# Kernel optimization log

Measured on AMD Instinct MI355X. Metric: run time of the kernel, lower is better.

Reference implementation:

```python
import jax, jax.numpy as jnp
import numpy as np

N, E = 50000, 800000
F_IN, H, P, C = 128, 64, 16, 40
L = 3  # gcn_layers


def setup_inputs() -> dict:
    key = jax.random.key(0)
    ks = jax.random.split(key, 10)
    s = 0.05
    return {
        "x_h": jax.random.normal(ks[0], (N, F_IN), jnp.float32),
        "pos_feat": jax.random.normal(ks[1], (N, P), jnp.float32),
        "edge_index": jax.random.randint(ks[2], (2, E), 0, N, dtype=jnp.int32),
        "W_pos": jax.random.normal(ks[3], (P, H), jnp.float32) * s,
        "b_pos": jnp.zeros((H,), jnp.float32),
        "W_init": jax.random.normal(ks[4], (F_IN, H), jnp.float32) * s,
        "b_init": jnp.zeros((H,), jnp.float32),
        "W_l": jax.random.normal(ks[5], (L, H, H), jnp.float32) * s,  # neighbor weight
        "W_r": jax.random.normal(ks[6], (L, H, H), jnp.float32) * s,  # root weight
        "b_conv": jnp.zeros((L, H), jnp.float32),
        "W_last": jax.random.normal(ks[7], (H, C), jnp.float32) * s,
        "b_last": jnp.zeros((C,), jnp.float32),
    }


def _sage_conv(x, src, dst, Wl, Wr, b):
    # PyG SAGEConv(aggr='mean'): out_i = Wl @ mean_{j in N(i)} x_j + Wr @ x_i + b
    msgs = x[src]  # [E, H] gather of source-node features
    agg = jax.ops.segment_sum(msgs, dst, num_segments=N)
    cnt = jax.ops.segment_sum(jnp.ones((E,), x.dtype), dst, num_segments=N)
    agg = agg / jnp.clip(cnt, 1.0, None)[:, None]  # mean; deg-0 nodes -> 0
    return agg @ Wl + x @ Wr + b


def reference(x_h, pos_feat, edge_index, W_pos, b_pos, W_init, b_init,
              W_l, W_r, b_conv, W_last, b_last):
    src, dst = edge_index[0], edge_index[1]
    # pos_embedding -> (hyperbolic encode simplified to identity in Euclidean manifold) -> tanh
    hyp_pos = jnp.tanh(pos_feat @ W_pos + b_pos)  # [N, H]
    h = x_h @ W_init + b_init  # [N, H]
    for i in range(L):
        h = _sage_conv(h, src, dst, W_l[i], W_r[i], b_conv[i])
        if i != L - 1:
            h = h + hyp_pos       # run_base == 'False' branch
            h = jax.nn.relu(h)    # dropout is no-op in eval mode
    emb = h @ W_last + b_last     # [N, C]
    return emb, jax.nn.log_softmax(emb, axis=1)
```

## Files before the change

### kernel.cpp

```cpp
#include <hip/hip_runtime.h>
#include <hip/hip_bf16.h>

#define NN 50000
#define NE 800000
#define FIN 128
#define HD 64
#define NC 40
#define XG   782
#define XG2  781
#define NB   391
#define NBK  782
#define BW   64
#define BSTR 2048

typedef __hip_bfloat16 bf16;
typedef __attribute__((ext_vector_type(8))) short bf16x8;
typedef __attribute__((ext_vector_type(4))) float f32x4;

__device__ __forceinline__ void acc8(float* a, uint4 v){
  a[0] += __uint_as_float(v.x << 16); a[1] += __uint_as_float(v.x & 0xffff0000u);
  a[2] += __uint_as_float(v.y << 16); a[3] += __uint_as_float(v.y & 0xffff0000u);
  a[4] += __uint_as_float(v.z << 16); a[5] += __uint_as_float(v.z & 0xffff0000u);
  a[6] += __uint_as_float(v.w << 16); a[7] += __uint_as_float(v.w & 0xffff0000u);
}

__device__ __forceinline__ unsigned pack2(float lo, float hi){
  union { bf16 b; unsigned short u; } a, b;
  a.b = __float2bfloat16(lo);
  b.b = __float2bfloat16(hi);
  return (unsigned)a.u | ((unsigned)b.u << 16);
}

__device__ __forceinline__ short f2bf_bits(float f){
  union { bf16 b; short s; } u;
  u.b = __float2bfloat16(f);
  return u.s;
}

__device__ __forceinline__ void init_body(
    int wid, const float* __restrict__ x, const float* __restrict__ pos,
    const float* __restrict__ Wi, const float* __restrict__ bi,
    const float* __restrict__ Wp, const float* __restrict__ bp,
    bf16* __restrict__ h0b, bf16* __restrict__ hypb, int lane){
  const int quad = lane >> 4;
  const int col  = lane & 15;
  const int nw   = XG * 4;

  bf16x8 wif[4][4];
  #pragma unroll
  for (int ct = 0; ct < 4; ++ct)
    #pragma unroll
    for (int kf = 0; kf < 4; ++kf)
      #pragma unroll
      for (int j = 0; j < 8; ++j)
        wif[ct][kf][j] = f2bf_bits(Wi[(kf*32 + quad*8 + j)*HD + ct*16 + col]);
  bf16x8 wpf[4];
  #pragma unroll
  for (int ct = 0; ct < 4; ++ct)
    #pragma unroll
    for (int j = 0; j < 8; ++j){
      const int k = quad*8 + j;
      wpf[ct][j] = (k < 16) ? f2bf_bits(Wp[k*HD + ct*16 + col]) : (short)0;
    }
  float bih[4], bph[4];
  #pragma unroll
  for (int c = 0; c < 4; ++c){ bih[c] = bi[c*16 + col]; bph[c] = bp[c*16 + col]; }

  for (int t = wid; t < NN/16; t += nw){
    const int n0 = t * 16;
    bf16x8 af[4];
    #pragma unroll
    for (int kf = 0; kf < 4; ++kf){
      const float* xr = x + (size_t)(n0 + col)*FIN + kf*32 + quad*8;
      const float4 f0 = *(const float4*)xr;
      const float4 f1 = *(const float4*)(xr + 4);
      af[kf][0] = f2bf_bits(f0.x); af[kf][1] = f2bf_bits(f0.y);
      af[kf][2] = f2bf_bits(f0.z); af[kf][3] = f2bf_bits(f0.w);
      af[kf][4] = f2bf_bits(f1.x); af[kf][5] = f2bf_bits(f1.y);
      af[kf][6] = f2bf_bits(f1.z); af[kf][7] = f2bf_bits(f1.w);
    }
    bf16x8 ap;
    #pragma unroll
    for (int j = 0; j < 8; ++j) ap[j] = 0;
    if (quad < 2){
      const float* pr = pos + (size_t)(n0 + col)*16 + quad*8;
      const float4 p0 = *(const float4*)pr;
      const float4 p1 = *(const float4*)(pr + 4);
      ap[0] = f2bf_bits(p0.x); ap[1] = f2bf_bits(p0.y);
      ap[2] = f2bf_bits(p0.z); ap[3] = f2bf_bits(p0.w);
      ap[4] = f2bf_bits(p1.x); ap[5] = f2bf_bits(p1.y);
      ap[6] = f2bf_bits(p1.z); ap[7] = f2bf_bits(p1.w);
    }
    f32x4 ah[4], app[4];
    #pragma unroll
    for (int c = 0; c < 4; ++c){
      ah[c]  = (f32x4){bih[c], bih[c], bih[c], bih[c]};
      app[c] = (f32x4){bph[c], bph[c], bph[c], bph[c]};
    }
    #pragma unroll
    for (int ct = 0; ct < 4; ++ct){
      #pragma unroll
      for (int kf = 0; kf < 4; ++kf)
        ah[ct] = __builtin_amdgcn_mfma_f32_16x16x32_bf16(af[kf], wif[ct][kf], ah[ct], 0, 0, 0);
      app[ct] = __builtin_amdgcn_mfma_f32_16x16x32_bf16(ap, wpf[ct], app[ct], 0, 0, 0);
    }
    #pragma unroll
    for (int reg = 0; reg < 4; ++reg){
      const int n = n0 + quad*4 + reg;
      #pragma unroll
      for (int c = 0; c < 4; ++c){
        h0b[(size_t)n*HD + c*16 + col]  = __float2bfloat16(ah[c][reg]);
        hypb[(size_t)n*HD + c*16 + col] = __float2bfloat16(tanhf(app[c][reg]));
      }
    }
  }
}

__device__ __forceinline__ void xform_body(
    int wid, int nw, const bf16* __restrict__ h, const float* __restrict__ Wl,
    const float* __restrict__ Wr, const float* __restrict__ bc,
    const bf16* __restrict__ hypb, const int use_hyp,
    bf16* __restrict__ y, bf16* __restrict__ z, int lane){
  const int quad = lane >> 4;
  const int col  = lane & 15;

  bf16x8 bfr[8][2];
  #pragma unroll
  for (int ct = 0; ct < 8; ++ct){
    const float* W = (ct < 4) ? Wl : Wr;
    const int nc = (ct & 3) * 16 + col;
    #pragma unroll
    for (int kf = 0; kf < 2; ++kf)
      #pragma unroll
      for (int j = 0; j < 8; ++j)
        bfr[ct][kf][j] = f2bf_bits(W[(kf*32 + quad*8 + j)*HD + nc]);
  }
  float zb[4];
  #pragma unroll
  for (int c = 0; c < 4; ++c) zb[c] = bc[c*16 + col];

  for (int t = wid; t < NN/16; t += nw){
    const int n0 = t * 16;
    union { uint4 u; bf16x8 v; } a0, a1;
    a0.u = *(const uint4*)(h + (size_t)(n0 + col)*HD + quad*8);
    a1.u = *(const uint4*)(h + (size_t)(n0 + col)*HD + 32 + quad*8);
    f32x4 acc[8];
    #pragma unroll
    for (int c = 0; c < 4; ++c) acc[c] = (f32x4){0.f, 0.f, 0.f, 0.f};
    #pragma unroll
    for (int c = 0; c < 4; ++c) acc[4+c] = (f32x4){zb[c], zb[c], zb[c], zb[c]};
    #pragma unroll
    for (int ct = 0; ct < 8; ++ct){
      acc[ct] = __builtin_amdgcn_mfma_f32_16x16x32_bf16(a0.v, bfr[ct][0], acc[ct], 0, 0, 0);
      acc[ct] = __builtin_amdgcn_mfma_f32_16x16x32_bf16(a1.v, bfr[ct][1], acc[ct], 0, 0, 0);
    }
    #pragma unroll
    for (int reg = 0; reg < 4; ++reg){
      const int n = n0 + quad*4 + reg;
      #pragma unroll
      for (int c = 0; c < 4; ++c){
        y[(size_t)n*HD + c*16 + col] = __float2bfloat16(acc[c][reg]);
        float zv = acc[4+c][reg];
        if (use_hyp) zv += __bfloat162float(hypb[(size_t)n*HD + c*16 + col]);
        z[(size_t)n*HD + c*16 + col] = __float2bfloat16(zv);
      }
    }
  }
}

__global__ __launch_bounds__(256) void k_hist(
    const int* __restrict__ ei, int* __restrict__ histT,
    const float* __restrict__ x, const float* __restrict__ pos,
    const float* __restrict__ Wi, const float* __restrict__ bi,
    const float* __restrict__ Wp, const float* __restrict__ bp,
    bf16* __restrict__ h0b, bf16* __restrict__ hypb){
  __shared__ int lh[NBK];
  if (blockIdx.x < NB){
    for (int i = threadIdx.x; i < NBK; i += 256) lh[i] = 0;
    __syncthreads();
    int e = blockIdx.x * 2048 + threadIdx.x;
    #pragma unroll
    for (int j = 0; j < 8; ++j, e += 256)
      if (e < NE) atomicAdd(&lh[ei[NE + e] >> 6], 1);
    __syncthreads();
    for (int i = threadIdx.x; i < NBK; i += 256)
      histT[blockIdx.x*NBK + i] = lh[i];
    return;
  }
  init_body((blockIdx.x - NB) * 4 + (threadIdx.x >> 6),
            x, pos, Wi, bi, Wp, bp, h0b, hypb, threadIdx.x & 63);
}

__global__ __launch_bounds__(512) void k_scanA(
    const int* __restrict__ histT, int* __restrict__ ofsT,
    int* __restrict__ totals){
  __shared__ int sc[512];
  const int b = blockIdx.x;
  const int t = threadIdx.x;
  const int v = (t < NB) ? histT[t*NBK + b] : 0;
  sc[t] = v; __syncthreads();
  for (int off = 1; off < 512; off <<= 1){
    const int xv = (t >= off) ? sc[t - off] : 0;
    __syncthreads();
    sc[t] += xv;
    __syncthreads();
  }
  if (t < NB) ofsT[t*NBK + b] = sc[t] - v;
  if (t == 511) totals[b] = sc[511];
}

__global__ __launch_bounds__(256) void k_scatter(
    const int* __restrict__ ei, const int* __restrict__ ofsT,
    int* __restrict__ packed){
  __shared__ int cur[NBK];
  for (int i = threadIdx.x; i < NBK; i += 256)
    cur[i] = (i << 11) + ofsT[blockIdx.x*NBK + i];
  __syncthreads();
  int e = blockIdx.x * 2048 + threadIdx.x;
  #pragma unroll
  for (int j = 0; j < 8; ++j, e += 256){
    if (e < NE){
      const int d = ei[NE + e];
      const int s = ei[e];
      const int b = d >> 6;
      const int p = atomicAdd(&cur[b], 1);
      if (p < ((b + 1) << 11))
        packed[p] = s | ((d & 63) << 16);
    }
  }
}

__global__ __launch_bounds__(256) void k_ellx(
    const int* __restrict__ packed, const int* __restrict__ totals,
    unsigned short* __restrict__ esrc, int* __restrict__ degp,
    const bf16* __restrict__ h0, const float* __restrict__ Wl,
    const float* __restrict__ Wr, const float* __restrict__ bc,
    const bf16* __restrict__ hypb, bf16* __restrict__ y, bf16* __restrict__ z){
  if (blockIdx.x < NBK){
    __shared__ int cnt[BW];
    __shared__ unsigned short ell[BW * 64];
    if (threadIdx.x < BW) cnt[threadIdx.x] = 0;
    __syncthreads();
    const int b  = blockIdx.x;
    const int lo = b << 11;
    const int hi = lo + totals[b];
    for (int e = lo + threadIdx.x; e < hi; e += 256){
      const int pk = packed[e];
      const int dl = (pk >> 16) & 63;
      const int p  = atomicAdd(&cnt[dl], 1);
      if (p < 64) ell[dl*64 + p] = (unsigned short)(pk & 0xffff);
    }
    __syncthreads();
    const int n0 = b * BW;
    for (int i = threadIdx.x; i < BW * 8; i += 256){
      const int node = i >> 3;
      if (n0 + node < NN)
        ((uint4*)(esrc + (size_t)(n0 + node)*64))[i & 7] = ((const uint4*)ell)[i];
    }
    for (int i = threadIdx.x; i < BW; i += 256)
      if (n0 + i < NN) degp[n0 + i] = cnt[i];
    return;
  }
  xform_body((blockIdx.x - NBK)*4 + (threadIdx.x >> 6), XG2*4,
             h0, Wl, Wr, bc, hypb, 1, y, z, threadIdx.x & 63);
}

__device__ __forceinline__ void gather_stage(
    const bf16* __restrict__ y, const bf16* __restrict__ z,
    const int* __restrict__ degp, const unsigned short* __restrict__ esrc,
    unsigned int* hs, const int do_relu){
  const int lane = threadIdx.x & 63;
  const int w    = threadIdx.x >> 6;
  const int grp  = lane >> 3;
  const int fq   = lane & 7;
  const int nl   = (w << 3) + grp;
  const int n    = (blockIdx.x << 5) + nl;
  const int ns   = (n < NN) ? n : 0;
  const int deg  = (n < NN) ? min(degp[n], 64) : 0;
  const uint4* er = (const uint4*)(esrc + ((size_t)ns << 6));
  float a[8] = {0,0,0,0,0,0,0,0};
  for (int eb = 0; eb < 64; eb += 8){
    if (!__any(eb < deg)) break;
    union { uint4 u; unsigned short s[8]; } ev;
    ev.u = er[eb >> 3];
    const int m = deg - eb;
    #pragma unroll
    for (int j = 0; j < 8; ++j){
      if (j < m){
        const uint4 v = ((const uint4*)(y + (size_t)ev.s[j]*HD))[fq];
        acc8(a, v);
      }
    }
  }
  const float inv = deg > 0 ? 1.f / (float)deg : 0.f;
  const uint4 zv = ((const uint4*)(z + (size_t)ns*HD))[fq];
  float zf[8];
  zf[0] = __uint_as_float(zv.x << 16); zf[1] = __uint_as_float(zv.x & 0xffff0000u);
  zf[2] = __uint_as_float(zv.y << 16); zf[3] = __uint_as_float(zv.y & 0xffff0000u);
  zf[4] = __uint_as_float(zv.z << 16); zf[5] = __uint_as_float(zv.z & 0xffff0000u);
  zf[6] = __uint_as_float(zv.w << 16); zf[7] = __uint_as_float(zv.w & 0xffff0000u);
  float o[8];
  #pragma unroll
  for (int j = 0; j < 8; ++j){
    o[j] = a[j]*inv + zf[j];
    if (do_relu) o[j] = fmaxf(o[j], 0.f);
  }
  uint4 pv;
  pv.x = pack2(o[0], o[1]);
  pv.y = pack2(o[2], o[3]);
  pv.z = pack2(o[4], o[5]);
  pv.w = pack2(o[6], o[7]);
  *(uint4*)(hs + nl*32 + ((fq ^ (nl & 7)) << 2)) = pv;
}

__device__ __forceinline__ bf16x8 lds_frag(const unsigned int* hs, int r, int slotlin){
  union { uint4 u; bf16x8 v; } t;
  t.u = *(const uint4*)(hs + r*32 + ((slotlin ^ (r & 7)) << 2));
  return t.v;
}

__global__ __launch_bounds__(256) void k_gx(
    const bf16* __restrict__ y, const bf16* __restrict__ z,
    const int* __restrict__ degp, const unsigned short* __restrict__ esrc,
    const float* __restrict__ Wl, const float* __restrict__ Wr,
    const float* __restrict__ bc, const bf16* __restrict__ hypb,
    const int use_hyp, bf16* __restrict__ yo, bf16* __restrict__ zo){
  __shared__ unsigned int hs[32*32];
  const int lane = threadIdx.x & 63;
  const int w    = threadIdx.x >> 6;
  const int quad = lane >> 4;
  const int col  = lane & 15;
  const int tile = w & 1;
  const int ch   = w >> 1;

  bf16x8 fl[2][2], fr[2][2];
  float zb[2];
  #pragma unroll
  for (int c = 0; c < 2; ++c){
    const int nc = (ch*2 + c)*16 + col;
    zb[c] = bc[nc];
    #pragma unroll
    for (int kf = 0; kf < 2; ++kf)
      #pragma unroll
      for (int j = 0; j < 8; ++j){
        fl[c][kf][j] = f2bf_bits(Wl[(kf*32 + quad*8 + j)*HD + nc]);
        fr[c][kf][j] = f2bf_bits(Wr[(kf*32 + quad*8 + j)*HD + nc]);
      }
  }

  gather_stage(y, z, degp, esrc, hs, 1);
  __syncthreads();

  const int r = tile*16 + col;
  const bf16x8 a0 = lds_frag(hs, r, quad);
  const bf16x8 a1 = lds_frag(hs, r, quad + 4);
  f32x4 ay[2], az[2];
  #pragma unroll
  for (int c = 0; c < 2; ++c){
    ay[c] = (f32x4){0.f, 0.f, 0.f, 0.f};
    az[c] = (f32x4){zb[c], zb[c], zb[c], zb[c]};
    ay[c] = __builtin_amdgcn_mfma_f32_16x16x32_bf16(a0, fl[c][0], ay[c], 0, 0, 0);
    ay[c] = __builtin_amdgcn_mfma_f32_16x16x32_bf16(a1, fl[c][1], ay[c], 0, 0, 0);
    az[c] = __builtin_amdgcn_mfma_f32_16x16x32_bf16(a0, fr[c][0], az[c], 0, 0, 0);
    az[c] = __builtin_amdgcn_mfma_f32_16x16x32_bf16(a1, fr[c][1], az[c], 0, 0, 0);
  }
  const int n0b = blockIdx.x << 5;
  #pragma unroll
  for (int reg = 0; reg < 4; ++reg){
    const int n = n0b + tile*16 + quad*4 + reg;
    if (n < NN){
      #pragma unroll
      for (int c = 0; c < 2; ++c){
        const int oc = (ch*2 + c)*16 + col;
        yo[(size_t)n*HD + oc] = __float2bfloat16(ay[c][reg]);
        float zv = az[c][reg];
        if (use_hyp) zv += __bfloat162float(hypb[(size_t)n*HD + oc]);
        zo[(size_t)n*HD + oc] = __float2bfloat16(zv);
      }
    }
  }
}

__global__ __launch_bounds__(256) void k_gf(
    const bf16* __restrict__ y, const bf16* __restrict__ z,
    const int* __restrict__ degp, const unsigned short* __restrict__ esrc,
    const float* __restrict__ Wl, const float* __restrict__ bl,
    float* __restrict__ out){
  __shared__ unsigned int hs[32*32];
  const int lane = threadIdx.x & 63;
  const int w    = threadIdx.x >> 6;
  const int quad = lane >> 4;
  const int col  = lane & 15;

  bf16x8 wf[3][2];
  float bb[3];
  #pragma unroll
  for (int ct = 0; ct < 3; ++ct){
    const int nc = ct*16 + col;
    const bool valid = nc < NC;
    bb[ct] = valid ? bl[nc] : -1e30f;
    #pragma unroll
    for (int kf = 0; kf < 2; ++kf)
      #pragma unroll
      for (int j = 0; j < 8; ++j)
        wf[ct][kf][j] = valid ? f2bf_bits(Wl[(kf*32 + quad*8 + j)*NC + nc]) : (short)0;
  }

  gather_stage(y, z, degp, esrc, hs, 0);
  __syncthreads();
  if (w >= 2) return;

  const int tile = w;
  const int r = tile*16 + col;
  const bf16x8 a0 = lds_frag(hs, r, quad);
  const bf16x8 a1 = lds_frag(hs, r, quad + 4);
  f32x4 acc[3];
  #pragma unroll
  for (int ct = 0; ct < 3; ++ct){
    acc[ct] = (f32x4){bb[ct], bb[ct], bb[ct], bb[ct]};
    acc[ct] = __builtin_amdgcn_mfma_f32_16x16x32_bf16(a0, wf[ct][0], acc[ct], 0, 0, 0);
    acc[ct] = __builtin_amdgcn_mfma_f32_16x16x32_bf16(a1, wf[ct][1], acc[ct], 0, 0, 0);
  }
  const int n0b = blockIdx.x << 5;
  #pragma unroll
  for (int reg = 0; reg < 4; ++reg){
    const float e0 = acc[0][reg], e1 = acc[1][reg], e2 = acc[2][reg];
    float vmax = fmaxf(fmaxf(e0, e1), e2);
    vmax = fmaxf(vmax, __shfl_xor(vmax, 1, 64));
    vmax = fmaxf(vmax, __shfl_xor(vmax, 2, 64));
    vmax = fmaxf(vmax, __shfl_xor(vmax, 4, 64));
    vmax = fmaxf(vmax, __shfl_xor(vmax, 8, 64));
    float s = __expf(e0 - vmax) + __expf(e1 - vmax) + __expf(e2 - vmax);
    s += __shfl_xor(s, 1, 64);
    s += __shfl_xor(s, 2, 64);
    s += __shfl_xor(s, 4, 64);
    s += __shfl_xor(s, 8, 64);
    const float off = vmax + __logf(s);
    const int n = n0b + tile*16 + quad*4 + reg;
    if (n < NN){
      #pragma unroll
      for (int ct = 0; ct < 3; ++ct){
        const int nc = ct*16 + col;
        if (nc < NC){
          const float e = acc[ct][reg];
          out[(size_t)n*NC + nc]                 = e;
          out[(size_t)NN*NC + (size_t)n*NC + nc] = e - off;
        }
      }
    }
  }
}

extern "C" void kernel_launch(void* const* d_in, const int* in_sizes, int n_in,
                              void* d_out, int out_size, void* d_ws, size_t ws_size,
                              hipStream_t stream){
  (void)in_sizes; (void)n_in; (void)out_size; (void)ws_size;
  const float* x_h    = (const float*)d_in[0];
  const float* pos    = (const float*)d_in[1];
  const int*   ei     = (const int*)  d_in[2];
  const float* W_pos  = (const float*)d_in[3];
  const float* b_pos  = (const float*)d_in[4];
  const float* W_init = (const float*)d_in[5];
  const float* b_init = (const float*)d_in[6];
  const float* W_l    = (const float*)d_in[7];
  const float* W_r    = (const float*)d_in[8];
  const float* b_conv = (const float*)d_in[9];
  const float* W_last = (const float*)d_in[10];
  const float* b_last = (const float*)d_in[11];
  float* out = (float*)d_out;

  char* p = (char*)d_ws;
  auto alloc = [&](size_t bytes)->char*{
    char* r = p; p += (bytes + 255) & ~(size_t)255; return r;
  };
  bf16* hb0  = (bf16*)alloc((size_t)NN*HD*2);
  bf16* y0   = (bf16*)alloc((size_t)NN*HD*2);
  bf16* z0   = (bf16*)alloc((size_t)NN*HD*2);
  bf16* y1   = (bf16*)alloc((size_t)NN*HD*2);
  bf16* z1   = (bf16*)alloc((size_t)NN*HD*2);
  bf16* hypb = (bf16*)alloc((size_t)NN*HD*2);
  unsigned short* esrc = (unsigned short*)alloc((size_t)NN*64*2);
  int* degp   = (int*)alloc((size_t)NN*4);
  int* histT  = (int*)alloc((size_t)NB*NBK*4);
  int* ofsT   = (int*)alloc((size_t)NB*NBK*4);
  int* totals = (int*)alloc((size_t)NBK*4);
  int* packed = (int*)alloc((size_t)NBK*BSTR*4);

  k_hist   <<<NB + XG, 256, 0, stream>>>(ei, histT, x_h, pos,
                                         W_init, b_init, W_pos, b_pos, hb0, hypb);
  k_scanA  <<<NBK, 512, 0, stream>>>(histT, ofsT, totals);
  k_scatter<<<NB, 256, 0, stream>>>(ei, ofsT, packed);
  k_ellx   <<<NBK + XG2, 256, 0, stream>>>(packed, totals, esrc, degp,
                                           hb0, W_l, W_r, b_conv, hypb, y0, z0);
  k_gx <<<1563, 256, 0, stream>>>(y0, z0, degp, esrc,
                                  W_l + 1*HD*HD, W_r + 1*HD*HD, b_conv + 1*HD,
                                  hypb, 1, y1, z1);
  k_gx <<<1563, 256, 0, stream>>>(y1, z1, degp, esrc,
                                  W_l + 2*HD*HD, W_r + 2*HD*HD, b_conv + 2*HD,
                                  hypb, 0, y0, z0);
  k_gf <<<1563, 256, 0, stream>>>(y0, z0, degp, esrc, W_last, b_last, out);
}
```

Baseline: 249.4 us.

## Aggregate raw features then apply fused concat GEMM instead of pre-transforming y/z

Reorders each SAGE layer to gather-mean the raw node features first, then run one MFMA GEMM over the concatenated [mean, self] row with stacked Wl/Wr, adding hyp and applying ReLU in the epilogue. This removes the separate y/z transform pass: each layer reads and writes one feature buffer instead of two, and the transform no longer sits in k_ellx. The final kernel also fuses the layer-3 conv with the output projection and log-softmax. The cost is a doubled K dimension in each block's GEMM, extra LDS staging, and another block-level barrier.

```diff
diff --git a/kernel.cpp b/kernel.cpp
--- a/kernel.cpp
+++ b/kernel.cpp
@@ -7,11 +7,11 @@
 #define HD 64
 #define NC 40
 #define XG   782
-#define XG2  781
 #define NB   391
 #define NBK  782
 #define BW   64
 #define BSTR 2048
+#define GGRID 1563
 
 typedef __hip_bfloat16 bf16;
 typedef __attribute__((ext_vector_type(8))) short bf16x8;
@@ -111,58 +111,6 @@
       for (int c = 0; c < 4; ++c){
         h0b[(size_t)n*HD + c*16 + col]  = __float2bfloat16(ah[c][reg]);
         hypb[(size_t)n*HD + c*16 + col] = __float2bfloat16(tanhf(app[c][reg]));
-      }
-    }
-  }
-}
-
-__device__ __forceinline__ void xform_body(
-    int wid, int nw, const bf16* __restrict__ h, const float* __restrict__ Wl,
-    const float* __restrict__ Wr, const float* __restrict__ bc,
-    const bf16* __restrict__ hypb, const int use_hyp,
-    bf16* __restrict__ y, bf16* __restrict__ z, int lane){
-  const int quad = lane >> 4;
-  const int col  = lane & 15;
-
-  bf16x8 bfr[8][2];
-  #pragma unroll
-  for (int ct = 0; ct < 8; ++ct){
-    const float* W = (ct < 4) ? Wl : Wr;
-    const int nc = (ct & 3) * 16 + col;
-    #pragma unroll
-    for (int kf = 0; kf < 2; ++kf)
-      #pragma unroll
-      for (int j = 0; j < 8; ++j)
-        bfr[ct][kf][j] = f2bf_bits(W[(kf*32 + quad*8 + j)*HD + nc]);
-  }
-  float zb[4];
-  #pragma unroll
-  for (int c = 0; c < 4; ++c) zb[c] = bc[c*16 + col];
-
-  for (int t = wid; t < NN/16; t += nw){
-    const int n0 = t * 16;
-    union { uint4 u; bf16x8 v; } a0, a1;
-    a0.u = *(const uint4*)(h + (size_t)(n0 + col)*HD + quad*8);
-    a1.u = *(const uint4*)(h + (size_t)(n0 + col)*HD + 32 + quad*8);
-    f32x4 acc[8];
-    #pragma unroll
-    for (int c = 0; c < 4; ++c) acc[c] = (f32x4){0.f, 0.f, 0.f, 0.f};
-    #pragma unroll
-    for (int c = 0; c < 4; ++c) acc[4+c] = (f32x4){zb[c], zb[c], zb[c], zb[c]};
-    #pragma unroll
-    for (int ct = 0; ct < 8; ++ct){
-      acc[ct] = __builtin_amdgcn_mfma_f32_16x16x32_bf16(a0.v, bfr[ct][0], acc[ct], 0, 0, 0);
-      acc[ct] = __builtin_amdgcn_mfma_f32_16x16x32_bf16(a1.v, bfr[ct][1], acc[ct], 0, 0, 0);
-    }
-    #pragma unroll
-    for (int reg = 0; reg < 4; ++reg){
-      const int n = n0 + quad*4 + reg;
-      #pragma unroll
-      for (int c = 0; c < 4; ++c){
-        y[(size_t)n*HD + c*16 + col] = __float2bfloat16(acc[c][reg]);
-        float zv = acc[4+c][reg];
-        if (use_hyp) zv += __bfloat162float(hypb[(size_t)n*HD + c*16 + col]);
-        z[(size_t)n*HD + c*16 + col] = __float2bfloat16(zv);
       }
     }
   }
@@ -230,45 +178,43 @@
   }
 }
 
-__global__ __launch_bounds__(256) void k_ellx(
+__global__ __launch_bounds__(256) void k_ell(
     const int* __restrict__ packed, const int* __restrict__ totals,
-    unsigned short* __restrict__ esrc, int* __restrict__ degp,
-    const bf16* __restrict__ h0, const float* __restrict__ Wl,
-    const float* __restrict__ Wr, const float* __restrict__ bc,
-    const bf16* __restrict__ hypb, bf16* __restrict__ y, bf16* __restrict__ z){
-  if (blockIdx.x < NBK){
-    __shared__ int cnt[BW];
-    __shared__ unsigned short ell[BW * 64];
-    if (threadIdx.x < BW) cnt[threadIdx.x] = 0;
-    __syncthreads();
-    const int b  = blockIdx.x;
-    const int lo = b << 11;
-    const int hi = lo + totals[b];
-    for (int e = lo + threadIdx.x; e < hi; e += 256){
-      const int pk = packed[e];
-      const int dl = (pk >> 16) & 63;
-      const int p  = atomicAdd(&cnt[dl], 1);
-      if (p < 64) ell[dl*64 + p] = (unsigned short)(pk & 0xffff);
-    }
-    __syncthreads();
-    const int n0 = b * BW;
-    for (int i = threadIdx.x; i < BW * 8; i += 256){
-      const int node = i >> 3;
-      if (n0 + node < NN)
-        ((uint4*)(esrc + (size_t)(n0 + node)*64))[i & 7] = ((const uint4*)ell)[i];
-    }
-    for (int i = threadIdx.x; i < BW; i += 256)
-      if (n0 + i < NN) degp[n0 + i] = cnt[i];
-    return;
-  }
-  xform_body((blockIdx.x - NBK)*4 + (threadIdx.x >> 6), XG2*4,
-             h0, Wl, Wr, bc, hypb, 1, y, z, threadIdx.x & 63);
-}
-
-__device__ __forceinline__ void gather_stage(
-    const bf16* __restrict__ y, const bf16* __restrict__ z,
-    const int* __restrict__ degp, const unsigned short* __restrict__ esrc,
-    unsigned int* hs, const int do_relu){
+    unsigned short* __restrict__ esrc, int* __restrict__ degp){
+  __shared__ int cnt[BW];
+  __shared__ unsigned short ell[BW * 64];
+  if (threadIdx.x < BW) cnt[threadIdx.x] = 0;
+  __syncthreads();
+  const int b  = blockIdx.x;
+  const int lo = b << 11;
+  const int hi = lo + totals[b];
+  for (int e = lo + threadIdx.x; e < hi; e += 256){
+    const int pk = packed[e];
+    const int dl = (pk >> 16) & 63;
+    const int p  = atomicAdd(&cnt[dl], 1);
+    if (p < 64) ell[dl*64 + p] = (unsigned short)(pk & 0xffff);
+  }
+  __syncthreads();
+  const int n0 = b * BW;
+  for (int i = threadIdx.x; i < BW * 8; i += 256){
+    const int node = i >> 3;
+    if (n0 + node < NN)
+      ((uint4*)(esrc + (size_t)(n0 + node)*64))[i & 7] = ((const uint4*)ell)[i];
+  }
+  for (int i = threadIdx.x; i < BW; i += 256)
+    if (n0 + i < NN) degp[n0 + i] = min(cnt[i], 64);
+}
+
+
+__device__ __forceinline__ bf16x8 lds_frag(const unsigned int* hs, int r, int slot){
+  union { uint4 u; bf16x8 v; } t;
+  t.u = *(const uint4*)(hs + r*32 + ((slot ^ (r & 7)) << 2));
+  return t.v;
+}
+
+__device__ __forceinline__ void gather_own_stage(
+    const bf16* __restrict__ h, const int* __restrict__ degp,
+    const unsigned short* __restrict__ esrc, unsigned int* hs){
   const int lane = threadIdx.x & 63;
   const int w    = threadIdx.x >> 6;
   const int grp  = lane >> 3;
@@ -277,6 +223,10 @@
   const int n    = (blockIdx.x << 5) + nl;
   const int ns   = (n < NN) ? n : 0;
   const int deg  = (n < NN) ? min(degp[n], 64) : 0;
+
+  const uint4 hv = ((const uint4*)(h + (size_t)ns*HD))[fq];
+  *(uint4*)(hs + 1024 + nl*32 + ((fq ^ (nl & 7)) << 2)) = hv;
+
   const uint4* er = (const uint4*)(esrc + ((size_t)ns << 6));
   float a[8] = {0,0,0,0,0,0,0,0};
   for (int eb = 0; eb < 64; eb += 8){
@@ -287,45 +237,27 @@
     #pragma unroll
     for (int j = 0; j < 8; ++j){
       if (j < m){
-        const uint4 v = ((const uint4*)(y + (size_t)ev.s[j]*HD))[fq];
+        const uint4 v = ((const uint4*)(h + (size_t)ev.s[j]*HD))[fq];
         acc8(a, v);
       }
     }
   }
   const float inv = deg > 0 ? 1.f / (float)deg : 0.f;
-  const uint4 zv = ((const uint4*)(z + (size_t)ns*HD))[fq];
-  float zf[8];
-  zf[0] = __uint_as_float(zv.x << 16); zf[1] = __uint_as_float(zv.x & 0xffff0000u);
-  zf[2] = __uint_as_float(zv.y << 16); zf[3] = __uint_as_float(zv.y & 0xffff0000u);
-  zf[4] = __uint_as_float(zv.z << 16); zf[5] = __uint_as_float(zv.z & 0xffff0000u);
-  zf[6] = __uint_as_float(zv.w << 16); zf[7] = __uint_as_float(zv.w & 0xffff0000u);
-  float o[8];
-  #pragma unroll
-  for (int j = 0; j < 8; ++j){
-    o[j] = a[j]*inv + zf[j];
-    if (do_relu) o[j] = fmaxf(o[j], 0.f);
-  }
   uint4 pv;
-  pv.x = pack2(o[0], o[1]);
-  pv.y = pack2(o[2], o[3]);
-  pv.z = pack2(o[4], o[5]);
-  pv.w = pack2(o[6], o[7]);
+  pv.x = pack2(a[0]*inv, a[1]*inv);
+  pv.y = pack2(a[2]*inv, a[3]*inv);
+  pv.z = pack2(a[4]*inv, a[5]*inv);
+  pv.w = pack2(a[6]*inv, a[7]*inv);
   *(uint4*)(hs + nl*32 + ((fq ^ (nl & 7)) << 2)) = pv;
 }
 
-__device__ __forceinline__ bf16x8 lds_frag(const unsigned int* hs, int r, int slotlin){
-  union { uint4 u; bf16x8 v; } t;
-  t.u = *(const uint4*)(hs + r*32 + ((slotlin ^ (r & 7)) << 2));
-  return t.v;
-}
-
-__global__ __launch_bounds__(256) void k_gx(
-    const bf16* __restrict__ y, const bf16* __restrict__ z,
-    const int* __restrict__ degp, const unsigned short* __restrict__ esrc,
+__global__ __launch_bounds__(256) void k_g(
+    const bf16* __restrict__ h, const int* __restrict__ degp,
+    const unsigned short* __restrict__ esrc,
     const float* __restrict__ Wl, const float* __restrict__ Wr,
     const float* __restrict__ bc, const bf16* __restrict__ hypb,
-    const int use_hyp, bf16* __restrict__ yo, bf16* __restrict__ zo){
-  __shared__ unsigned int hs[32*32];
+    bf16* __restrict__ ho){
+  __shared__ unsigned int hs[2048];
   const int lane = threadIdx.x & 63;
   const int w    = threadIdx.x >> 6;
   const int quad = lane >> 4;
@@ -333,64 +265,127 @@
   const int tile = w & 1;
   const int ch   = w >> 1;
 
-  bf16x8 fl[2][2], fr[2][2];
+  bf16x8 fw[2][4];
   float zb[2];
   #pragma unroll
   for (int c = 0; c < 2; ++c){
     const int nc = (ch*2 + c)*16 + col;
     zb[c] = bc[nc];
     #pragma unroll
-    for (int kf = 0; kf < 2; ++kf)
+    for (int kf = 0; kf < 4; ++kf)
       #pragma unroll
       for (int j = 0; j < 8; ++j){
-        fl[c][kf][j] = f2bf_bits(Wl[(kf*32 + quad*8 + j)*HD + nc]);
-        fr[c][kf][j] = f2bf_bits(Wr[(kf*32 + quad*8 + j)*HD + nc]);
+        const int k = kf*32 + quad*8 + j;
+        fw[c][kf][j] = f2bf_bits((k < 64) ? Wl[k*HD + nc] : Wr[(k - 64)*HD + nc]);
       }
   }
 
-  gather_stage(y, z, degp, esrc, hs, 1);
+  gather_own_stage(h, degp, esrc, hs);
   __syncthreads();
 
   const int r = tile*16 + col;
   const bf16x8 a0 = lds_frag(hs, r, quad);
   const bf16x8 a1 = lds_frag(hs, r, quad + 4);
-  f32x4 ay[2], az[2];
+  const bf16x8 a2 = lds_frag(hs + 1024, r, quad);
+  const bf16x8 a3 = lds_frag(hs + 1024, r, quad + 4);
+  __syncthreads();
+
+  const int n0b = blockIdx.x << 5;
+  unsigned short* st = (unsigned short*)hs;
+  f32x4 acc[2];
   #pragma unroll
   for (int c = 0; c < 2; ++c){
-    ay[c] = (f32x4){0.f, 0.f, 0.f, 0.f};
-    az[c] = (f32x4){zb[c], zb[c], zb[c], zb[c]};
-    ay[c] = __builtin_amdgcn_mfma_f32_16x16x32_bf16(a0, fl[c][0], ay[c], 0, 0, 0);
-    ay[c] = __builtin_amdgcn_mfma_f32_16x16x32_bf16(a1, fl[c][1], ay[c], 0, 0, 0);
-    az[c] = __builtin_amdgcn_mfma_f32_16x16x32_bf16(a0, fr[c][0], az[c], 0, 0, 0);
-    az[c] = __builtin_amdgcn_mfma_f32_16x16x32_bf16(a1, fr[c][1], az[c], 0, 0, 0);
-  }
-  const int n0b = blockIdx.x << 5;
+    acc[c] = (f32x4){zb[c], zb[c], zb[c], zb[c]};
+    acc[c] = __builtin_amdgcn_mfma_f32_16x16x32_bf16(a0, fw[c][0], acc[c], 0, 0, 0);
+    acc[c] = __builtin_amdgcn_mfma_f32_16x16x32_bf16(a1, fw[c][1], acc[c], 0, 0, 0);
+    acc[c] = __builtin_amdgcn_mfma_f32_16x16x32_bf16(a2, fw[c][2], acc[c], 0, 0, 0);
+    acc[c] = __builtin_amdgcn_mfma_f32_16x16x32_bf16(a3, fw[c][3], acc[c], 0, 0, 0);
+  }
   #pragma unroll
   for (int reg = 0; reg < 4; ++reg){
-    const int n = n0b + tile*16 + quad*4 + reg;
-    if (n < NN){
-      #pragma unroll
-      for (int c = 0; c < 2; ++c){
-        const int oc = (ch*2 + c)*16 + col;
-        yo[(size_t)n*HD + oc] = __float2bfloat16(ay[c][reg]);
-        float zv = az[c][reg];
-        if (use_hyp) zv += __bfloat162float(hypb[(size_t)n*HD + oc]);
-        zo[(size_t)n*HD + oc] = __float2bfloat16(zv);
-      }
-    }
-  }
+    const int rr = tile*16 + quad*4 + reg;
+    const int nn = n0b + rr;
+    #pragma unroll
+    for (int c = 0; c < 2; ++c){
+      const int oc = (ch*2 + c)*16 + col;
+      float v = acc[c][reg];
+      if (nn < NN) v += __bfloat162float(hypb[(size_t)nn*HD + oc]);
+      v = fmaxf(v, 0.f);
+      st[rr*64 + (((oc >> 3) ^ (rr & 7)) << 3) + (oc & 7)] = (unsigned short)f2bf_bits(v);
+    }
+  }
+  __syncthreads();
+  const int grp = lane >> 3;
+  const int fq  = lane & 7;
+  const int nl  = (w << 3) + grp;
+  const int n   = n0b + nl;
+  if (n < NN)
+    ((uint4*)(ho + (size_t)n*HD))[fq] = *(const uint4*)(hs + nl*32 + ((fq ^ (nl & 7)) << 2));
 }
 
 __global__ __launch_bounds__(256) void k_gf(
-    const bf16* __restrict__ y, const bf16* __restrict__ z,
-    const int* __restrict__ degp, const unsigned short* __restrict__ esrc,
-    const float* __restrict__ Wl, const float* __restrict__ bl,
+    const bf16* __restrict__ h, const int* __restrict__ degp,
+    const unsigned short* __restrict__ esrc,
+    const float* __restrict__ Wl, const float* __restrict__ Wr,
+    const float* __restrict__ bc,
+    const float* __restrict__ Wlast, const float* __restrict__ blast,
     float* __restrict__ out){
-  __shared__ unsigned int hs[32*32];
+  __shared__ unsigned int hs[2048];
   const int lane = threadIdx.x & 63;
   const int w    = threadIdx.x >> 6;
   const int quad = lane >> 4;
   const int col  = lane & 15;
+  const int tile = w & 1;
+  const int ch   = w >> 1;
+
+  bf16x8 fw[2][4];
+  float zb[2];
+  #pragma unroll
+  for (int c = 0; c < 2; ++c){
+    const int nc = (ch*2 + c)*16 + col;
+    zb[c] = bc[nc];
+    #pragma unroll
+    for (int kf = 0; kf < 4; ++kf)
+      #pragma unroll
+      for (int j = 0; j < 8; ++j){
+        const int k = kf*32 + quad*8 + j;
+        fw[c][kf][j] = f2bf_bits((k < 64) ? Wl[k*HD + nc] : Wr[(k - 64)*HD + nc]);
+      }
+  }
+
+  gather_own_stage(h, degp, esrc, hs);
+  __syncthreads();
+
+  const int r = tile*16 + col;
+  const bf16x8 a0 = lds_frag(hs, r, quad);
+  const bf16x8 a1 = lds_frag(hs, r, quad + 4);
+  const bf16x8 a2 = lds_frag(hs + 1024, r, quad);
+  const bf16x8 a3 = lds_frag(hs + 1024, r, quad + 4);
+  __syncthreads();
+
+  const int n0b = blockIdx.x << 5;
+  unsigned short* st = (unsigned short*)hs;
+  f32x4 acc[2];
+  #pragma unroll
+  for (int c = 0; c < 2; ++c){
+    acc[c] = (f32x4){zb[c], zb[c], zb[c], zb[c]};
+    acc[c] = __builtin_amdgcn_mfma_f32_16x16x32_bf16(a0, fw[c][0], acc[c], 0, 0, 0);
+    acc[c] = __builtin_amdgcn_mfma_f32_16x16x32_bf16(a1, fw[c][1], acc[c], 0, 0, 0);
+    acc[c] = __builtin_amdgcn_mfma_f32_16x16x32_bf16(a2, fw[c][2], acc[c], 0, 0, 0);
+    acc[c] = __builtin_amdgcn_mfma_f32_16x16x32_bf16(a3, fw[c][3], acc[c], 0, 0, 0);
+  }
+  #pragma unroll
+  for (int reg = 0; reg < 4; ++reg){
+    const int rr = tile*16 + quad*4 + reg;
+    #pragma unroll
+    for (int c = 0; c < 2; ++c){
+      const int oc = (ch*2 + c)*16 + col;
+      st[rr*64 + (((oc >> 3) ^ (rr & 7)) << 3) + (oc & 7)] =
+          (unsigned short)f2bf_bits(acc[c][reg]);
+    }
+  }
+  __syncthreads();
+  if (w >= 2) return;
 
   bf16x8 wf[3][2];
   float bb[3];
@@ -398,33 +393,26 @@
   for (int ct = 0; ct < 3; ++ct){
     const int nc = ct*16 + col;
     const bool valid = nc < NC;
-    bb[ct] = valid ? bl[nc] : -1e30f;
+    bb[ct] = valid ? blast[nc] : -1e30f;
     #pragma unroll
     for (int kf = 0; kf < 2; ++kf)
       #pragma unroll
       for (int j = 0; j < 8; ++j)
-        wf[ct][kf][j] = valid ? f2bf_bits(Wl[(kf*32 + quad*8 + j)*NC + nc]) : (short)0;
-  }
-
-  gather_stage(y, z, degp, esrc, hs, 0);
-  __syncthreads();
-  if (w >= 2) return;
-
-  const int tile = w;
-  const int r = tile*16 + col;
-  const bf16x8 a0 = lds_frag(hs, r, quad);
-  const bf16x8 a1 = lds_frag(hs, r, quad + 4);
-  f32x4 acc[3];
+        wf[ct][kf][j] = valid ? f2bf_bits(Wlast[(kf*32 + quad*8 + j)*NC + nc]) : (short)0;
+  }
+  const int r2 = w*16 + col;
+  const bf16x8 b0 = lds_frag(hs, r2, quad);
+  const bf16x8 b1 = lds_frag(hs, r2, quad + 4);
+  f32x4 ac[3];
   #pragma unroll
   for (int ct = 0; ct < 3; ++ct){
-    acc[ct] = (f32x4){bb[ct], bb[ct], bb[ct], bb[ct]};
-    acc[ct] = __builtin_amdgcn_mfma_f32_16x16x32_bf16(a0, wf[ct][0], acc[ct], 0, 0, 0);
-    acc[ct] = __builtin_amdgcn_mfma_f32_16x16x32_bf16(a1, wf[ct][1], acc[ct], 0, 0, 0);
-  }
-  const int n0b = blockIdx.x << 5;
+    ac[ct] = (f32x4){bb[ct], bb[ct], bb[ct], bb[ct]};
+    ac[ct] = __builtin_amdgcn_mfma_f32_16x16x32_bf16(b0, wf[ct][0], ac[ct], 0, 0, 0);
+    ac[ct] = __builtin_amdgcn_mfma_f32_16x16x32_bf16(b1, wf[ct][1], ac[ct], 0, 0, 0);
+  }
   #pragma unroll
   for (int reg = 0; reg < 4; ++reg){
-    const float e0 = acc[0][reg], e1 = acc[1][reg], e2 = acc[2][reg];
+    const float e0 = ac[0][reg], e1 = ac[1][reg], e2 = ac[2][reg];
     float vmax = fmaxf(fmaxf(e0, e1), e2);
     vmax = fmaxf(vmax, __shfl_xor(vmax, 1, 64));
     vmax = fmaxf(vmax, __shfl_xor(vmax, 2, 64));
@@ -436,13 +424,13 @@
     s += __shfl_xor(s, 4, 64);
     s += __shfl_xor(s, 8, 64);
     const float off = vmax + __logf(s);
-    const int n = n0b + tile*16 + quad*4 + reg;
+    const int n = n0b + w*16 + quad*4 + reg;
     if (n < NN){
       #pragma unroll
       for (int ct = 0; ct < 3; ++ct){
         const int nc = ct*16 + col;
         if (nc < NC){
-          const float e = acc[ct][reg];
+          const float e = ac[ct][reg];
           out[(size_t)n*NC + nc]                 = e;
           out[(size_t)NN*NC + (size_t)n*NC + nc] = e - off;
         }
@@ -473,11 +461,8 @@
   auto alloc = [&](size_t bytes)->char*{
     char* r = p; p += (bytes + 255) & ~(size_t)255; return r;
   };
-  bf16* hb0  = (bf16*)alloc((size_t)NN*HD*2);
-  bf16* y0   = (bf16*)alloc((size_t)NN*HD*2);
-  bf16* z0   = (bf16*)alloc((size_t)NN*HD*2);
-  bf16* y1   = (bf16*)alloc((size_t)NN*HD*2);
-  bf16* z1   = (bf16*)alloc((size_t)NN*HD*2);
+  bf16* buf0 = (bf16*)alloc((size_t)NN*HD*2);
+  bf16* buf1 = (bf16*)alloc((size_t)NN*HD*2);
   bf16* hypb = (bf16*)alloc((size_t)NN*HD*2);
   unsigned short* esrc = (unsigned short*)alloc((size_t)NN*64*2);
   int* degp   = (int*)alloc((size_t)NN*4);
@@ -487,16 +472,18 @@
   int* packed = (int*)alloc((size_t)NBK*BSTR*4);
 
   k_hist   <<<NB + XG, 256, 0, stream>>>(ei, histT, x_h, pos,
-                                         W_init, b_init, W_pos, b_pos, hb0, hypb);
+                                         W_init, b_init, W_pos, b_pos, buf0, hypb);
   k_scanA  <<<NBK, 512, 0, stream>>>(histT, ofsT, totals);
   k_scatter<<<NB, 256, 0, stream>>>(ei, ofsT, packed);
-  k_ellx   <<<NBK + XG2, 256, 0, stream>>>(packed, totals, esrc, degp,
-                                           hb0, W_l, W_r, b_conv, hypb, y0, z0);
-  k_gx <<<1563, 256, 0, stream>>>(y0, z0, degp, esrc,
-                                  W_l + 1*HD*HD, W_r + 1*HD*HD, b_conv + 1*HD,
-                                  hypb, 1, y1, z1);
-  k_gx <<<1563, 256, 0, stream>>>(y1, z1, degp, esrc,
-                                  W_l + 2*HD*HD, W_r + 2*HD*HD, b_conv + 2*HD,
-                                  hypb, 0, y0, z0);
-  k_gf <<<1563, 256, 0, stream>>>(y0, z0, degp, esrc, W_last, b_last, out);
-}
+  k_ell    <<<NBK, 256, 0, stream>>>(packed, totals, esrc, degp);
+
+  k_g  <<<GGRID, 256, 0, stream>>>(buf0, degp, esrc,
+                                   W_l + 0*HD*HD, W_r + 0*HD*HD, b_conv + 0*HD,
+                                   hypb, buf1);
+  k_g  <<<GGRID, 256, 0, stream>>>(buf1, degp, esrc,
+                                   W_l + 1*HD*HD, W_r + 1*HD*HD, b_conv + 1*HD,
+                                   hypb, buf0);
+  k_gf <<<GGRID, 256, 0, stream>>>(buf0, degp, esrc,
+                                   W_l + 2*HD*HD, W_r + 2*HD*HD, b_conv + 2*HD,
+                                   W_last, b_last, out);
+}
```

Result: faster. 240.7 us (-3.5%).
